# Kernel optimization log

Measured on AMD Instinct MI355X. Metric: run time of the kernel, lower is better.

The kernel has to match this reference:

```python
import jax, jax.numpy as jnp
import numpy as np

N_NODES = 100000
N_EDGES = 1600000
N_GRAPHS = 64
IN_C, HID, OUT_C = 9, 128, 2


def setup_inputs() -> dict:
    key = jax.random.key(0)
    ks = jax.random.split(key, 10)
    x = jax.random.normal(ks[0], (N_NODES, IN_C), dtype=jnp.float32)
    edge_index = jax.random.randint(ks[1], (2, N_EDGES), 0, N_NODES, dtype=jnp.int64)
    batch = jnp.sort(jax.random.randint(ks[2], (N_NODES,), 0, N_GRAPHS, dtype=jnp.int64))
    # GCNConv params (glorot-ish scale) and biases
    W1 = jax.random.normal(ks[3], (IN_C, HID), dtype=jnp.float32) / np.sqrt(IN_C)
    b1 = jnp.zeros((HID,), dtype=jnp.float32)
    W2 = jax.random.normal(ks[4], (HID, HID), dtype=jnp.float32) / np.sqrt(HID)
    b2 = jnp.zeros((HID,), dtype=jnp.float32)
    Wc = jax.random.normal(ks[5], (HID, OUT_C), dtype=jnp.float32) / np.sqrt(HID)
    bc = jnp.zeros((OUT_C,), dtype=jnp.float32)
    return {"x": x, "edge_index": edge_index, "batch": batch,
            "W1": W1, "b1": b1, "W2": W2, "b2": b2, "Wc": Wc, "bc": bc}


def _gcn_conv(x, row, col, dinv, W, b):
    # x: [N, Fin] -> [N, Fout]; symmetric-normalized scatter-add over edges+self-loops
    xw = x @ W                                   # dense GEMM
    norm = dinv[row] * dinv[col]                 # [E+N]
    msg = xw[row] * norm[:, None]                # gather + scale
    out = jax.ops.segment_sum(msg, col, num_segments=x.shape[0])  # scatter-add at target
    return out + b


def reference(x, edge_index, batch, W1, b1, W2, b2, Wc, bc):
    n = x.shape[0]
    loops = jnp.arange(n, dtype=edge_index.dtype)
    row = jnp.concatenate([edge_index[0], loops])  # sources (with self-loops)
    col = jnp.concatenate([edge_index[1], loops])  # targets
    deg = jax.ops.segment_sum(jnp.ones_like(col, dtype=x.dtype), col, num_segments=n)
    dinv = jnp.where(deg > 0, jax.lax.rsqrt(deg), 0.0)
    h = jax.nn.relu(_gcn_conv(x, row, col, dinv, W1, b1))
    h = jax.nn.relu(_gcn_conv(h, row, col, dinv, W2, b2))
    # global mean pool over graphs
    sums = jax.ops.segment_sum(h, batch, num_segments=N_GRAPHS)
    cnts = jax.ops.segment_sum(jnp.ones((n,), dtype=h.dtype), batch, num_segments=N_GRAPHS)
    pooled = sums / jnp.maximum(cnts, 1.0)[:, None]
    return pooled @ Wc + bc
```

## Files before the change

kernel.cpp:

```cpp
#include <hip/hip_runtime.h>

#define NN 100000
#define NE 1600000
#define NG 64
#define HIDC 128
#define INC 9
#define OUTC 2
#define BSH 9
#define NBK ((NN + 511) / 512)
#define EPB 4096
#define NBLKA ((NE + EPB - 1) / EPB)
#define CAP 12288

typedef unsigned int u32;

#define PACK_REC(lc, r) (((u32)(lc) << 17) | (u32)(r))
#define REC_LC(v) ((v) >> 17)
#define REC_ROW(v) ((v) & 0x1FFFFu)

__device__ inline float bf_lo(u32 u) { return __uint_as_float(u << 16); }
__device__ inline float bf_hi(u32 u) { return __uint_as_float(u & 0xFFFF0000u); }
__device__ inline u32 f2bf(float x) {
    u32 u = __float_as_uint(x);
    return (u + 0x7FFFu + ((u >> 16) & 1u)) >> 16;
}
__device__ inline u32 packbf(float a, float b) { return f2bf(a) | (f2bf(b) << 16); }

__global__ void k_zero196(int* bcnt) {
    int t = threadIdx.x;
    if (t < NBK) bcnt[t] = 0;
}

__global__ __launch_bounds__(256) void k_bscatter2(const int* __restrict__ row,
                                                   const int* __restrict__ col,
                                                   int* bcnt, u32* __restrict__ staging) {
    __shared__ u32 srec[EPB];
    __shared__ u32 sbkt[EPB];
    __shared__ int hist[NBK];
    __shared__ int base[NBK];
    int t = threadIdx.x;
    long e0 = (long)blockIdx.x * EPB;
    int n = (NE - e0 < EPB) ? (int)(NE - e0) : EPB;
    for (int i = t; i < n; i += 256) {
        u32 c = col[e0 + i];
        u32 r = row[e0 + i];
        srec[i] = PACK_REC(c & 511u, r);
        sbkt[i] = c >> BSH;
    }
    if (t < NBK) hist[t] = 0;
    __syncthreads();
    for (int i = t; i < n; i += 256) atomicAdd(&hist[sbkt[i]], 1);
    __syncthreads();
    if (t < NBK) {
        int h = hist[t];
        base[t] = h ? atomicAdd(&bcnt[t], h) : 0;
        hist[t] = 0;
    }
    __syncthreads();
    for (int i = t; i < n; i += 256) {
        int b = sbkt[i];
        int p = atomicAdd(&hist[b], 1) + base[b];
        if (p < CAP) staging[(long)b * CAP + p] = srec[i];
    }
}

__global__ __launch_bounds__(256) void k_bscan(const int* __restrict__ bcnt,
                                               int* __restrict__ bbase,
                                               int* __restrict__ offsets) {
    __shared__ int lds[256];
    int t = threadIdx.x;
    int v = (t < NBK) ? bcnt[t] : 0;
    lds[t] = v;
    __syncthreads();
    for (int d = 1; d < 256; d <<= 1) {
        int u = (t >= d) ? lds[t - d] : 0;
        __syncthreads();
        lds[t] += u;
        __syncthreads();
    }
    if (t < NBK) bbase[t] = lds[t] - v;
    if (t == 0) offsets[NN] = NE;
}

__global__ __launch_bounds__(256) void k_bcsr(const u32* __restrict__ staging,
                                              const int* __restrict__ bcnt,
                                              const int* __restrict__ bbase,
                                              int* __restrict__ offsets,
                                              float* __restrict__ dinv,
                                              int* __restrict__ csr_src) {
    __shared__ int cnt[512];
    __shared__ int cur[512];
    __shared__ int sc[256];
    int b = blockIdx.x, t = threadIdx.x;
    int nb0 = b << BSH;
    int nodes = NN - nb0 < 512 ? NN - nb0 : 512;
    int ne_b = bcnt[b];
    long s0b = (long)b * CAP;
    int e0 = bbase[b];
    cnt[t] = 0;
    cnt[t + 256] = 0;
    __syncthreads();
    for (int e = t; e < ne_b; e += 256)
        atomicAdd(&cnt[REC_LC(staging[s0b + e])], 1);
    __syncthreads();
    int c0 = cnt[2 * t], c1 = cnt[2 * t + 1];
    int s = c0 + c1;
    sc[t] = s;
    __syncthreads();
    for (int d = 1; d < 256; d <<= 1) {
        int u = (t >= d) ? sc[t - d] : 0;
        __syncthreads();
        sc[t] += u;
        __syncthreads();
    }
    int ex = sc[t] - s;
    cur[2 * t] = ex;
    cur[2 * t + 1] = ex + c0;
    if (2 * t < nodes) {
        offsets[nb0 + 2 * t] = e0 + ex;
        dinv[nb0 + 2 * t] = rsqrtf((float)(c0 + 1));
    }
    if (2 * t + 1 < nodes) {
        offsets[nb0 + 2 * t + 1] = e0 + ex + c0;
        dinv[nb0 + 2 * t + 1] = rsqrtf((float)(c1 + 1));
    }
    __syncthreads();
    for (int e = t; e < ne_b; e += 256) {
        u32 r = staging[s0b + e];
        int p = atomicAdd(&cur[REC_LC(r)], 1);
        csr_src[e0 + p] = (int)REC_ROW(r);
    }
}

__global__ __launch_bounds__(256) void k_xw1(const float* __restrict__ x,
                                             const float* __restrict__ W1,
                                             const float* __restrict__ dinv,
                                             u32* __restrict__ Ap2) {
    int tid = threadIdx.x;
    int i = blockIdx.x * 4 + (tid >> 6);
    int j = tid & 63;
    if (i >= NN) return;
    float acc0 = 0.f, acc1 = 0.f;
#pragma unroll
    for (int k = 0; k < INC; ++k) {
        float xv = x[i * INC + k];
        acc0 += xv * W1[k * HIDC + 2 * j];
        acc1 += xv * W1[k * HIDC + 2 * j + 1];
    }
    float di = dinv[i];
    Ap2[(long)i * 64 + j] = packbf(acc0 * di, acc1 * di);
}

__global__ __launch_bounds__(256) void k_gather(const u32* __restrict__ Ap2,
                                                const int* __restrict__ csr_src,
                                                const int* __restrict__ offsets,
                                                const float* __restrict__ dinv,
                                                u32* __restrict__ B2) {
    int i = (blockIdx.x * 256 + threadIdx.x) >> 6;
    if (i >= NN) return;
    int lane = threadIdx.x & 63;
    long base = (long)i * 64 + lane;
    u32 a = Ap2[base];
    float acc0 = bf_lo(a), acc1 = bf_hi(a);
    int beg = offsets[i], end = offsets[i + 1];
    int e = beg;
    for (; e + 8 <= end; e += 8) {
        int s0 = csr_src[e + 0], s1 = csr_src[e + 1], s2 = csr_src[e + 2], s3 = csr_src[e + 3];
        int s4 = csr_src[e + 4], s5 = csr_src[e + 5], s6 = csr_src[e + 6], s7 = csr_src[e + 7];
        u32 v0 = Ap2[(long)s0 * 64 + lane];
        u32 v1 = Ap2[(long)s1 * 64 + lane];
        u32 v2 = Ap2[(long)s2 * 64 + lane];
        u32 v3 = Ap2[(long)s3 * 64 + lane];
        u32 v4 = Ap2[(long)s4 * 64 + lane];
        u32 v5 = Ap2[(long)s5 * 64 + lane];
        u32 v6 = Ap2[(long)s6 * 64 + lane];
        u32 v7 = Ap2[(long)s7 * 64 + lane];
        acc0 += ((bf_lo(v0) + bf_lo(v1)) + (bf_lo(v2) + bf_lo(v3))) +
                ((bf_lo(v4) + bf_lo(v5)) + (bf_lo(v6) + bf_lo(v7)));
        acc1 += ((bf_hi(v0) + bf_hi(v1)) + (bf_hi(v2) + bf_hi(v3))) +
                ((bf_hi(v4) + bf_hi(v5)) + (bf_hi(v6) + bf_hi(v7)));
    }
    for (; e + 2 <= end; e += 2) {
        int s0 = csr_src[e], s1 = csr_src[e + 1];
        u32 v0 = Ap2[(long)s0 * 64 + lane];
        u32 v1 = Ap2[(long)s1 * 64 + lane];
        acc0 += bf_lo(v0) + bf_lo(v1);
        acc1 += bf_hi(v0) + bf_hi(v1);
    }
    for (; e < end; ++e) {
        u32 v = Ap2[(long)csr_src[e] * 64 + lane];
        acc0 += bf_lo(v);
        acc1 += bf_hi(v);
    }
    float di = dinv[i];
    B2[base] = packbf(acc0 * di, acc1 * di);
}

__global__ __launch_bounds__(256) void k_layer2(const u32* __restrict__ B2,
                                                const float* __restrict__ b1,
                                                const float* __restrict__ W2,
                                                const float* __restrict__ dinv,
                                                u32* __restrict__ Ap2) {
    __shared__ float hs[128][HIDC];
    int t = threadIdx.x;
    int nb = blockIdx.x * 128;
    int j = t & 63;
    float bb0 = b1[2 * j], bb1 = b1[2 * j + 1];
    for (int n = t >> 6; n < 128; n += 4) {
        int node = nb + n;
        u32 u = (node < NN) ? B2[(long)node * 64 + j] : 0u;
        float h0 = bf_lo(u) + bb0;
        float h1 = bf_hi(u) + bb1;
        hs[n][2 * j] = h0 > 0.f ? h0 : 0.f;
        hs[n][2 * j + 1] = h1 > 0.f ? h1 : 0.f;
    }
    __syncthreads();
    int cg = t & 7, ng = t >> 3;
    int n0 = ng * 4;
    const float4* W4 = (const float4*)W2;
    float acc[4][16] = {};
#pragma unroll 2
    for (int k = 0; k < HIDC; ++k) {
        float4 w0 = W4[k * 32 + cg * 4 + 0];
        float4 w1 = W4[k * 32 + cg * 4 + 1];
        float4 w2 = W4[k * 32 + cg * 4 + 2];
        float4 w3 = W4[k * 32 + cg * 4 + 3];
        float a0 = hs[n0 + 0][k], a1 = hs[n0 + 1][k];
        float a2 = hs[n0 + 2][k], a3 = hs[n0 + 3][k];
#pragma unroll
        for (int r = 0; r < 4; ++r) {
            float ar = (r == 0) ? a0 : (r == 1) ? a1 : (r == 2) ? a2 : a3;
            acc[r][0] += ar * w0.x;  acc[r][1] += ar * w0.y;  acc[r][2] += ar * w0.z;  acc[r][3] += ar * w0.w;
            acc[r][4] += ar * w1.x;  acc[r][5] += ar * w1.y;  acc[r][6] += ar * w1.z;  acc[r][7] += ar * w1.w;
            acc[r][8] += ar * w2.x;  acc[r][9] += ar * w2.y;  acc[r][10] += ar * w2.z; acc[r][11] += ar * w2.w;
            acc[r][12] += ar * w3.x; acc[r][13] += ar * w3.y; acc[r][14] += ar * w3.z; acc[r][15] += ar * w3.w;
        }
    }
#pragma unroll
    for (int r = 0; r < 4; ++r) {
        int node = nb + n0 + r;
        if (node < NN) {
            float di = dinv[node];
            uint4 oa, ob;
            oa.x = packbf(acc[r][0] * di, acc[r][1] * di);
            oa.y = packbf(acc[r][2] * di, acc[r][3] * di);
            oa.z = packbf(acc[r][4] * di, acc[r][5] * di);
            oa.w = packbf(acc[r][6] * di, acc[r][7] * di);
            ob.x = packbf(acc[r][8] * di, acc[r][9] * di);
            ob.y = packbf(acc[r][10] * di, acc[r][11] * di);
            ob.z = packbf(acc[r][12] * di, acc[r][13] * di);
            ob.w = packbf(acc[r][14] * di, acc[r][15] * di);
            ((uint4*)Ap2)[(long)node * 16 + cg * 2 + 0] = oa;
            ((uint4*)Ap2)[(long)node * 16 + cg * 2 + 1] = ob;
        }
    }
}

__global__ void k_pool_init(float* pooled, float* cnt) {
    int i = blockIdx.x * 256 + threadIdx.x;
    if (i < NG * HIDC) pooled[i] = 0.f;
    if (i < NG) cnt[i] = 0.f;
}

__global__ __launch_bounds__(64) void k_pool(const u32* __restrict__ B2,
                                             const float* __restrict__ b2,
                                             const int* __restrict__ batch,
                                             float* pooled, float* cnt) {
    int f = threadIdx.x;
    int start = blockIdx.x * 64;
    int end = start + 64 < NN ? start + 64 : NN;
    float bb0 = b2[2 * f], bb1 = b2[2 * f + 1];
    float s0 = 0.f, s1 = 0.f;
    int gcur = -1, cl = 0;
    for (int i = start; i < end; ++i) {
        int g = batch[i];
        if (g != gcur) {
            if (gcur >= 0) {
                unsafeAtomicAdd(&pooled[gcur * HIDC + 2 * f], s0);
                unsafeAtomicAdd(&pooled[gcur * HIDC + 2 * f + 1], s1);
                if (f == 0) unsafeAtomicAdd(&cnt[gcur], (float)cl);
            }
            gcur = g; s0 = s1 = 0.f; cl = 0;
        }
        u32 u = B2[(long)i * 64 + f];
        float h0 = bf_lo(u) + bb0;
        float h1 = bf_hi(u) + bb1;
        s0 += h0 > 0.f ? h0 : 0.f;
        s1 += h1 > 0.f ? h1 : 0.f;
        cl++;
    }
    if (gcur >= 0) {
        unsafeAtomicAdd(&pooled[gcur * HIDC + 2 * f], s0);
        unsafeAtomicAdd(&pooled[gcur * HIDC + 2 * f + 1], s1);
        if (f == 0) unsafeAtomicAdd(&cnt[gcur], (float)cl);
    }
}

__global__ __launch_bounds__(128) void k_final(const float* __restrict__ pooled,
                                               const float* __restrict__ cnt,
                                               const float* __restrict__ Wc,
                                               const float* __restrict__ bc,
                                               float* __restrict__ out) {
    __shared__ float v0s[HIDC], v1s[HIDC];
    int g = blockIdx.x, f = threadIdx.x;
    float c = cnt[g]; c = c > 1.f ? c : 1.f;
    float val = pooled[g * HIDC + f] / c;
    v0s[f] = val * Wc[f * OUTC + 0];
    v1s[f] = val * Wc[f * OUTC + 1];
    __syncthreads();
    if (f < 2) {
        const float* arr = (f == 0) ? v0s : v1s;
        float s = 0.f;
        for (int k = 0; k < HIDC; ++k) s += arr[k];
        out[g * OUTC + f] = s + bc[f];
    }
}

extern "C" void kernel_launch(void* const* d_in, const int* in_sizes, int n_in,
                              void* d_out, int out_size, void* d_ws, size_t ws_size,
                              hipStream_t stream) {
    const float* x     = (const float*)d_in[0];
    const int*   ei    = (const int*)d_in[1];
    const int*   batch = (const int*)d_in[2];
    const float* W1    = (const float*)d_in[3];
    const float* b1    = (const float*)d_in[4];
    const float* W2    = (const float*)d_in[5];
    const float* b2    = (const float*)d_in[6];
    const float* Wc    = (const float*)d_in[7];
    const float* bc    = (const float*)d_in[8];
    float* out = (float*)d_out;

    char* ws = (char*)d_ws;
    size_t off = 0;
    auto alloc = [&](size_t bytes) { void* p = ws + off; off += (bytes + 255) / 256 * 256; return p; };
    u32*   Ap2     = (u32*)alloc((size_t)NN * 64 * 4);
    u32*   B2      = (u32*)alloc((size_t)NN * 64 * 4);
    float* dinv    = (float*)alloc((size_t)NN * 4);
    int*   offsets = (int*)alloc((size_t)(NN + 1) * 4);
    int*   csr_src = (int*)alloc((size_t)NE * 4);
    u32*   staging = (u32*)alloc((size_t)NBK * CAP * 4);
    int*   bcnt    = (int*)alloc((size_t)NBK * 4);
    int*   bbase   = (int*)alloc((size_t)NBK * 4);
    float* pooled  = (float*)alloc((size_t)NG * HIDC * 4);
    float* cnt     = (float*)alloc((size_t)NG * 4);

    const int* row = ei;
    const int* col = ei + NE;

    k_zero196<<<1, 256, 0, stream>>>(bcnt);
    k_bscatter2<<<NBLKA, 256, 0, stream>>>(row, col, bcnt, staging);
    k_bscan<<<1, 256, 0, stream>>>(bcnt, bbase, offsets);
    k_bcsr<<<NBK, 256, 0, stream>>>(staging, bcnt, bbase, offsets, dinv, csr_src);

    k_xw1<<<(NN + 3) / 4, 256, 0, stream>>>(x, W1, dinv, Ap2);
    k_gather<<<(NN * 64 + 255) / 256, 256, 0, stream>>>(Ap2, csr_src, offsets, dinv, B2);

    k_layer2<<<(NN + 127) / 128, 256, 0, stream>>>(B2, b1, W2, dinv, Ap2);
    k_gather<<<(NN * 64 + 255) / 256, 256, 0, stream>>>(Ap2, csr_src, offsets, dinv, B2);

    k_pool_init<<<(NG * HIDC + 255) / 256, 256, 0, stream>>>(pooled, cnt);
    k_pool<<<(NN + 63) / 64, 64, 0, stream>>>(B2, b2, batch, pooled, cnt);
    k_final<<<NG, 128, 0, stream>>>(pooled, cnt, Wc, bc, out);
}
```

Before: 387.7 us.

## Stage W2 tiles in shared memory and shrink layer-2 GEMM node tile

```diff
diff --git a/kernel.cpp b/kernel.cpp
--- a/kernel.cpp
+++ b/kernel.cpp
@@ -201,12 +201,13 @@
                                                 const float* __restrict__ W2,
                                                 const float* __restrict__ dinv,
                                                 u32* __restrict__ Ap2) {
-    __shared__ float hs[128][HIDC];
+    __shared__ float hs[64][HIDC + 1];
+    __shared__ float W2s[32][HIDC];
     int t = threadIdx.x;
-    int nb = blockIdx.x * 128;
+    int nb = blockIdx.x * 64;
     int j = t & 63;
     float bb0 = b1[2 * j], bb1 = b1[2 * j + 1];
-    for (int n = t >> 6; n < 128; n += 4) {
+    for (int n = t >> 6; n < 64; n += 4) {
         int node = nb + n;
         u32 u = (node < NN) ? B2[(long)node * 64 + j] : 0u;
         float h0 = bf_lo(u) + bb0;
@@ -214,26 +215,29 @@
         hs[n][2 * j] = h0 > 0.f ? h0 : 0.f;
         hs[n][2 * j + 1] = h1 > 0.f ? h1 : 0.f;
     }
-    __syncthreads();
-    int cg = t & 7, ng = t >> 3;
-    int n0 = ng * 4;
-    const float4* W4 = (const float4*)W2;
-    float acc[4][16] = {};
-#pragma unroll 2
-    for (int k = 0; k < HIDC; ++k) {
-        float4 w0 = W4[k * 32 + cg * 4 + 0];
-        float4 w1 = W4[k * 32 + cg * 4 + 1];
-        float4 w2 = W4[k * 32 + cg * 4 + 2];
-        float4 w3 = W4[k * 32 + cg * 4 + 3];
-        float a0 = hs[n0 + 0][k], a1 = hs[n0 + 1][k];
-        float a2 = hs[n0 + 2][k], a3 = hs[n0 + 3][k];
-#pragma unroll
-        for (int r = 0; r < 4; ++r) {
-            float ar = (r == 0) ? a0 : (r == 1) ? a1 : (r == 2) ? a2 : a3;
-            acc[r][0] += ar * w0.x;  acc[r][1] += ar * w0.y;  acc[r][2] += ar * w0.z;  acc[r][3] += ar * w0.w;
-            acc[r][4] += ar * w1.x;  acc[r][5] += ar * w1.y;  acc[r][6] += ar * w1.z;  acc[r][7] += ar * w1.w;
-            acc[r][8] += ar * w2.x;  acc[r][9] += ar * w2.y;  acc[r][10] += ar * w2.z; acc[r][11] += ar * w2.w;
-            acc[r][12] += ar * w3.x; acc[r][13] += ar * w3.y; acc[r][14] += ar * w3.z; acc[r][15] += ar * w3.w;
+    int cg = t & 15, ng = t >> 4;
+    int n0 = ng * 4, c0 = cg * 4;
+    float acc[4][8] = {};
+    for (int kt = 0; kt < 4; ++kt) {
+        __syncthreads();
+        for (int idx = t; idx < 1024; idx += 256)
+            ((float4*)W2s)[idx] = ((const float4*)W2)[kt * 1024 + idx];
+        __syncthreads();
+#pragma unroll 8
+        for (int k = 0; k < 32; ++k) {
+            int kk = kt * 32 + k;
+            float a0 = hs[n0 + 0][kk], a1 = hs[n0 + 1][kk];
+            float a2 = hs[n0 + 2][kk], a3 = hs[n0 + 3][kk];
+            float4 w0 = *(const float4*)&W2s[k][c0];
+            float4 w1 = *(const float4*)&W2s[k][c0 + 64];
+            acc[0][0] += a0 * w0.x; acc[0][1] += a0 * w0.y; acc[0][2] += a0 * w0.z; acc[0][3] += a0 * w0.w;
+            acc[0][4] += a0 * w1.x; acc[0][5] += a0 * w1.y; acc[0][6] += a0 * w1.z; acc[0][7] += a0 * w1.w;
+            acc[1][0] += a1 * w0.x; acc[1][1] += a1 * w0.y; acc[1][2] += a1 * w0.z; acc[1][3] += a1 * w0.w;
+            acc[1][4] += a1 * w1.x; acc[1][5] += a1 * w1.y; acc[1][6] += a1 * w1.z; acc[1][7] += a1 * w1.w;
+            acc[2][0] += a2 * w0.x; acc[2][1] += a2 * w0.y; acc[2][2] += a2 * w0.z; acc[2][3] += a2 * w0.w;
+            acc[2][4] += a2 * w1.x; acc[2][5] += a2 * w1.y; acc[2][6] += a2 * w1.z; acc[2][7] += a2 * w1.w;
+            acc[3][0] += a3 * w0.x; acc[3][1] += a3 * w0.y; acc[3][2] += a3 * w0.z; acc[3][3] += a3 * w0.w;
+            acc[3][4] += a3 * w1.x; acc[3][5] += a3 * w1.y; acc[3][6] += a3 * w1.z; acc[3][7] += a3 * w1.w;
         }
     }
 #pragma unroll
@@ -241,17 +245,13 @@
         int node = nb + n0 + r;
         if (node < NN) {
             float di = dinv[node];
-            uint4 oa, ob;
+            uint2 oa, ob;
             oa.x = packbf(acc[r][0] * di, acc[r][1] * di);
             oa.y = packbf(acc[r][2] * di, acc[r][3] * di);
-            oa.z = packbf(acc[r][4] * di, acc[r][5] * di);
-            oa.w = packbf(acc[r][6] * di, acc[r][7] * di);
-            ob.x = packbf(acc[r][8] * di, acc[r][9] * di);
-            ob.y = packbf(acc[r][10] * di, acc[r][11] * di);
-            ob.z = packbf(acc[r][12] * di, acc[r][13] * di);
-            ob.w = packbf(acc[r][14] * di, acc[r][15] * di);
-            ((uint4*)Ap2)[(long)node * 16 + cg * 2 + 0] = oa;
-            ((uint4*)Ap2)[(long)node * 16 + cg * 2 + 1] = ob;
+            ob.x = packbf(acc[r][4] * di, acc[r][5] * di);
+            ob.y = packbf(acc[r][6] * di, acc[r][7] * di);
+            ((uint2*)Ap2)[(long)node * 32 + cg] = oa;
+            ((uint2*)Ap2)[(long)node * 32 + 16 + cg] = ob;
         }
     }
 }
@@ -355,7 +355,7 @@
     k_xw1<<<(NN + 3) / 4, 256, 0, stream>>>(x, W1, dinv, Ap2);
     k_gather<<<(NN * 64 + 255) / 256, 256, 0, stream>>>(Ap2, csr_src, offsets, dinv, B2);
 
-    k_layer2<<<(NN + 127) / 128, 256, 0, stream>>>(B2, b1, W2, dinv, Ap2);
+    k_layer2<<<(NN + 63) / 64, 256, 0, stream>>>(B2, b1, W2, dinv, Ap2);
     k_gather<<<(NN * 64 + 255) / 256, 256, 0, stream>>>(Ap2, csr_src, offsets, dinv, B2);
 
     k_pool_init<<<(NG * HIDC + 255) / 256, 256, 0, stream>>>(pooled, cnt);
```

After: 311.3 us. 1.25x faster.
